# Kernel tuning notes

Hardware: AMD Instinct MI355X
Metric: run time of the kernel (lower is better)

## Reference

```python
import jax, jax.numpy as jnp
import numpy as np

NG, NC = 4096, 4096
FIN_G, FIN_C, D = 512, 512, 256
ALPHA = 0.2
NEG = -9.0e15

def leaky(x):
    return jnp.where(x >= 0, x, ALPHA * x)

def setup_inputs() -> dict:
    key = jax.random.key(0)
    ks = jax.random.split(key, 16)
    gene_x = jax.random.normal(ks[0], (NG, FIN_G), jnp.float32)
    cell_x = jax.random.normal(ks[1], (NC, FIN_C), jnp.float32)
    gene_adj = (jax.random.uniform(ks[2], (NG, NG)) < 0.05).astype(jnp.float32)
    gene_adj = jnp.maximum(gene_adj, jnp.eye(NG, dtype=jnp.float32))
    cell_adj = (jax.random.uniform(ks[3], (NC, NC)) < 0.05).astype(jnp.float32)
    cell_adj = jnp.maximum(cell_adj, jnp.eye(NC, dtype=jnp.float32))
    gene_cell_adj = (jax.random.uniform(ks[4], (NG, NC)) < 0.05).astype(jnp.float32)
    s = 1.414 * np.sqrt(6.0)
    def xav(k, shape):
        lim = s / np.sqrt(shape[0] + shape[1])
        return jax.random.uniform(k, shape, jnp.float32, -lim, lim)
    Wg = xav(ks[5], (D, FIN_G))
    Wc = xav(ks[6], (D, FIN_C))
    a_gg = xav(ks[7], (2 * D, 1))
    a_gc = xav(ks[8], (2 * D, 1))
    a_cc = xav(ks[9], (2 * D, 1))
    a_cg = xav(ks[10], (2 * D, 1))
    gate_g_w = xav(ks[11], (1, D))
    gate_c_w = xav(ks[12], (1, D))
    gate_g_b = jnp.full((1,), -2.0, jnp.float32)
    gate_c_b = jnp.full((1,), -2.0, jnp.float32)
    return dict(gene_x=gene_x, cell_x=cell_x, gene_adj=gene_adj, cell_adj=cell_adj,
                gene_cell_adj=gene_cell_adj, Wg=Wg, Wc=Wc, a_gg=a_gg, a_gc=a_gc,
                a_cc=a_cc, a_cg=a_cg, gate_g_w=gate_g_w, gate_g_b=gate_g_b,
                gate_c_w=gate_c_w, gate_c_b=gate_c_b)

def _gat_block(src_h, dst_h, a, adj):
    # attention of src rows over dst columns; adj: [Ns, Nd]
    d = src_h.shape[1]
    s1 = src_h @ a[:d, :]          # [Ns,1]
    s2 = dst_h @ a[d:, :]          # [Nd,1]
    e = leaky(s1 + s2.T)           # [Ns,Nd]
    att = jax.nn.softmax(jnp.where(adj > 0, e, NEG), axis=1)
    return att @ dst_h             # [Ns,d]

def reference(gene_x, cell_x, gene_adj, cell_adj, gene_cell_adj,
              Wg, Wc, a_gg, a_gc, a_cc, a_cg,
              gate_g_w, gate_g_b, gate_c_w, gate_c_b):
    gene_h = gene_x @ Wg.T   # [Ng,D]
    cell_h = cell_x @ Wc.T   # [Nc,D]
    gene_from_gene = _gat_block(gene_h, gene_h, a_gg, gene_adj)
    gene_from_cell = _gat_block(gene_h, cell_h, a_gc, gene_cell_adj)
    cell_from_cell = _gat_block(cell_h, cell_h, a_cc, cell_adj)
    cell_from_gene = _gat_block(cell_h, gene_h, a_cg, gene_cell_adj.T)
    gamma_g = jax.nn.sigmoid(gene_h @ gate_g_w.T + gate_g_b)  # [Ng,1]
    gamma_c = jax.nn.sigmoid(cell_h @ gate_c_w.T + gate_c_b)  # [Nc,1]
    gene_out = leaky(gene_h + gene_from_gene + gamma_g * gene_from_cell)
    cell_out = leaky(cell_h + cell_from_cell + gamma_c * cell_from_gene)
    return gene_out, cell_out
```

## Files before the change

kernel.cpp:

```cpp
#include <hip/hip_runtime.h>
#include <stdint.h>

#define NGC 4096
#define FIN 512
#define DD  256

typedef __attribute__((ext_vector_type(8))) short short8;
typedef __attribute__((ext_vector_type(4))) float f32x4;
typedef unsigned short u16;
typedef unsigned int   u32;
typedef unsigned long long u64;

static __device__ __forceinline__ float bf2f(u16 u){ return __uint_as_float(((u32)u)<<16); }
static __device__ __forceinline__ u16 f2bf(float f){
  u32 u = __float_as_uint(f);
  u += 0x7fffu + ((u>>16)&1u);
  return (u16)(u>>16);
}
static __device__ __forceinline__ u64 pack4bf(f32x4 v){
  u64 r;
  r  = (u64)f2bf(v[0]);
  r |= (u64)f2bf(v[1]) << 16;
  r |= (u64)f2bf(v[2]) << 32;
  r |= (u64)f2bf(v[3]) << 48;
  return r;
}
static __device__ __forceinline__ float lk(float x){ return fmaxf(x, 0.2f*x); }
static __device__ __forceinline__ u64 shfl_xor64(u64 x, int m){
  u32 lo = (u32)x, hi = (u32)(x >> 32);
  lo = __shfl_xor(lo, m); hi = __shfl_xor(hi, m);
  return ((u64)hi << 32) | lo;
}
static __device__ __forceinline__ u64 spread4(u64 x){
  x &= 0xFFFFull;
  x = (x | (x << 24)) & 0x000000FF000000FFull;
  x = (x | (x << 12)) & 0x000F000F000F000Full;
  x = (x | (x << 6))  & 0x0303030303030303ull;
  x = (x | (x << 3))  & 0x1111111111111111ull;
  return x;
}
static __device__ __forceinline__ void gl16(const void* g, void* l){
  __builtin_amdgcn_global_load_lds(
    (const __attribute__((address_space(1))) void*)g,
    (__attribute__((address_space(3))) void*)l, 16, 0, 0);
}

__global__ __launch_bounds__(256) void k_wcvt(
    const float* __restrict__ Wg, const float* __restrict__ Wc,
    u16* __restrict__ Wgbf, u16* __restrict__ Wcbf)
{
  int base = (blockIdx.x*256 + threadIdx.x)*4;
  float4 a = *(const float4*)(Wg + base);
  float4 b = *(const float4*)(Wc + base);
  ushort4 oa, ob;
  oa.x=f2bf(a.x); oa.y=f2bf(a.y); oa.z=f2bf(a.z); oa.w=f2bf(a.w);
  ob.x=f2bf(b.x); ob.y=f2bf(b.y); ob.z=f2bf(b.z); ob.w=f2bf(b.w);
  *(ushort4*)(Wgbf + base) = oa;
  *(ushort4*)(Wcbf + base) = ob;
}

__global__ __launch_bounds__(256) void k_pack(
    const float* __restrict__ gene_adj, const float* __restrict__ cell_adj,
    const float* __restrict__ gc_adj,   u64* __restrict__ packbits)
{
  int t = threadIdx.x, wid = t>>6, lane = t&63;
  int w = blockIdx.x*4 + wid;
  int row0 = w*6;
  const int sel = lane >> 2;
  const int sh = (lane & 3) * 16;

  float4 bufA[16], bufB[16];

  {
    int m = row0 >> 12;
    const float* sp = (m==0) ? gene_adj : (m==1) ? cell_adj : gc_adj;
    const float* rp = sp + (size_t)(row0 & 4095)*NGC + lane*4;
    #pragma unroll
    for(int j=0;j<16;j++) bufA[j] = *(const float4*)(rp + j*256);
  }

  #pragma unroll
  for(int i=0;i<6;i++){
    const bool evn = (i & 1) == 0;
    if(i < 5){
      int row = row0 + i + 1;
      int m = row >> 12;
      const float* sp = (m==0) ? gene_adj : (m==1) ? cell_adj : gc_adj;
      const float* rp = sp + (size_t)(row & 4095)*NGC + lane*4;
      if(evn){
        #pragma unroll
        for(int j=0;j<16;j++) bufB[j] = *(const float4*)(rp + j*256);
      } else {
        #pragma unroll
        for(int j=0;j<16;j++) bufA[j] = *(const float4*)(rp + j*256);
      }
    }
    u64 k0=0, k1=0, k2=0, k3=0;
    #pragma unroll
    for(int j=0;j<16;j++){
      float4 v = evn ? bufA[j] : bufB[j];
      u64 b0 = __ballot(v.x != 0.0f);
      u64 b1 = __ballot(v.y != 0.0f);
      u64 b2 = __ballot(v.z != 0.0f);
      u64 b3 = __ballot(v.w != 0.0f);
      if(sel == j){ k0=b0; k1=b1; k2=b2; k3=b3; }
    }
    u64 wv = spread4(k0 >> sh) | (spread4(k1 >> sh) << 1)
           | (spread4(k2 >> sh) << 2) | (spread4(k3 >> sh) << 3);
    int row = row0 + i;
    packbits[((size_t)(row >> 12) << 18) + (size_t)(row & 4095)*64 + lane] = wv;
  }
}

__global__ __launch_bounds__(256) void k_bitTT(
    const u64* __restrict__ gcb, u64* __restrict__ bT)
{
  int t = threadIdx.x, wid = t>>6, lane = t&63;
  int id = blockIdx.x*4 + wid;
  int G = id & 63, C = id >> 6;

  u64 x = gcb[(size_t)(64*G + lane)*64 + C];

  const u64 M1  = 0xAAAAAAAAAAAAAAAAull;
  const u64 M2  = 0xCCCCCCCCCCCCCCCCull;
  const u64 M4  = 0xF0F0F0F0F0F0F0F0ull;
  const u64 M8  = 0xFF00FF00FF00FF00ull;
  const u64 M16 = 0xFFFF0000FFFF0000ull;
  const u64 M32 = 0xFFFFFFFF00000000ull;
  #define TSTEP(S, M) { u64 y = shfl_xor64(x, S); \
    x = (lane & S) ? ((x & (M)) | ((y >> S) & ~(M))) \
                   : ((x & ~(M)) | ((y << S) & (M))); }
  TSTEP(32, M32) TSTEP(16, M16) TSTEP(8, M8)
  TSTEP(4,  M4)  TSTEP(2,  M2)  TSTEP(1, M1)
  #undef TSTEP

  bT[(size_t)(64*C + lane)*64 + G] = x;
}

__global__ __launch_bounds__(512) void k_hgemm(
    const float* __restrict__ xg, const float* __restrict__ xc,
    const u16* __restrict__ Wg, const u16* __restrict__ Wc,
    float* __restrict__ hg, float* __restrict__ hc,
    u16* __restrict__ hTg, u16* __restrict__ hTc)
{
  const int side = blockIdx.y;
  const float* x = side ? xc : xg;
  const u16* W = side ? Wc : Wg;
  float* h  = side ? hc : hg;
  u16*  hT  = side ? hTc : hTg;
  const int r0 = blockIdx.x * 64;
  const int t = threadIdx.x;
  const int wid = t >> 6, lane = t & 63;
  const int lrow = lane & 15, lhi = lane >> 4;

  __shared__ __align__(16) char smem[32768];

  f32x4 acc[4][2];
  const f32x4 z4 = {0.f,0.f,0.f,0.f};
  #pragma unroll
  for(int i=0;i<4;i++){ acc[i][0]=z4; acc[i][1]=z4; }

  const int r = t >> 3, c8 = t & 7;
  for(int k0 = 0; k0 < FIN; k0 += 64){
    const float* xp = x + (size_t)(r0 + r)*FIN + k0 + c8*8;
    float4 xa = *(const float4*)xp;
    float4 xb = *(const float4*)(xp + 4);
    short8 xv;
    xv[0]=(short)f2bf(xa.x); xv[1]=(short)f2bf(xa.y);
    xv[2]=(short)f2bf(xa.z); xv[3]=(short)f2bf(xa.w);
    xv[4]=(short)f2bf(xb.x); xv[5]=(short)f2bf(xb.y);
    xv[6]=(short)f2bf(xb.z); xv[7]=(short)f2bf(xb.w);
    int wbyte = r*128 + (((c8 ^ (r & 7)) & 7) << 4);
    *(short8*)(smem + wbyte) = xv;
    __syncthreads();
    #pragma unroll
    for(int ksub = 0; ksub < 2; ksub++){
      short8 b[2];
      #pragma unroll
      for(int nf=0; nf<2; nf++){
        int n = wid*32 + nf*16 + lrow;
        b[nf] = *(const short8*)(W + (size_t)n*FIN + k0 + ksub*32 + lhi*8);
      }
      #pragma unroll
      for(int mf=0; mf<4; mf++){
        int row = mf*16 + lrow;
        int g = ksub*4 + lhi;
        short8 a = *(const short8*)(smem + row*128 + (((g ^ (row & 7)) & 7) << 4));
        #pragma unroll
        for(int nf=0; nf<2; nf++)
          acc[mf][nf] = __builtin_amdgcn_mfma_f32_16x16x32_bf16(a, b[nf], acc[mf][nf], 0,0,0);
      }
    }
    __syncthreads();
  }
  #pragma unroll
  for(int mf=0; mf<4; mf++){
    #pragma unroll
    for(int nf=0; nf<2; nf++){
      int col = wid*32 + nf*16 + lrow;
      #pragma unroll
      for(int j=0;j<4;j++){
        int row = mf*16 + lhi*4 + j;
        float v = acc[mf][nf][j];
        h[(size_t)(r0+row)*DD + col] = v;
        int byte_ = col*128 + (((row*2) ^ ((col & 7)<<4)));
        *(u16*)(smem + byte_) = f2bf(v);
      }
    }
  }
  __syncthreads();
  {
    int n = t >> 1, half = t & 1;
    #pragma unroll
    for(int gi=0; gi<4; gi++){
      int g = half*4 + gi;
      int byte_ = n*128 + (((g ^ (n & 7)) & 7) << 4);
      short8 v = *(const short8*)(smem + byte_);
      int kcol = r0 + g*8;
      size_t off = (size_t)(kcol>>5)*8192 + (size_t)(n>>4)*512
                 + ((kcol>>3)&3)*128 + (n&15)*8;
      *(short8*)(hT + off) = v;
    }
  }
}

__global__ __launch_bounds__(256) void k_svec(
    const float* __restrict__ hg, const float* __restrict__ hc,
    const float* __restrict__ a_gg, const float* __restrict__ a_gc,
    const float* __restrict__ a_cc, const float* __restrict__ a_cg,
    const float* __restrict__ gw_g, const float* __restrict__ gb_g,
    const float* __restrict__ gw_c, const float* __restrict__ gb_c,
    float* __restrict__ sbuf)
{
  int t = threadIdx.x, wid = t>>6, lane = t&63;
  int idx = blockIdx.x * 4 + wid;
  int side = idx >> 12;
  int row  = idx & 4095;
  const float* h = (side ? hc : hg) + (size_t)row*DD;
  const float* v0 = (side ? a_cc : a_gg);
  const float* v1 = (side ? a_cc : a_gg) + DD;
  const float* v2 = (side ? a_cg : a_gc);
  const float* v3 = (side ? a_gc : a_cg) + DD;
  const float* gw = side ? gw_c : gw_g;
  float bias = (side ? gb_c : gb_g)[0];

  float4 hv = *(const float4*)(h + lane*4);
  float4 w0 = *(const float4*)(v0 + lane*4);
  float4 w1 = *(const float4*)(v1 + lane*4);
  float4 w2 = *(const float4*)(v2 + lane*4);
  float4 w3 = *(const float4*)(v3 + lane*4);
  float4 w4 = *(const float4*)(gw + lane*4);

  float d0 = hv.x*w0.x + hv.y*w0.y + hv.z*w0.z + hv.w*w0.w;
  float d1 = hv.x*w1.x + hv.y*w1.y + hv.z*w1.z + hv.w*w1.w;
  float d2 = hv.x*w2.x + hv.y*w2.y + hv.z*w2.z + hv.w*w2.w;
  float d3 = hv.x*w3.x + hv.y*w3.y + hv.z*w3.z + hv.w*w3.w;
  float d4 = hv.x*w4.x + hv.y*w4.y + hv.z*w4.z + hv.w*w4.w;
  #pragma unroll
  for(int s=1;s<64;s<<=1){
    d0 += __shfl_xor(d0, s); d1 += __shfl_xor(d1, s); d2 += __shfl_xor(d2, s);
    d3 += __shfl_xor(d3, s); d4 += __shfl_xor(d4, s);
  }
  if(lane == 0){
    float gam = 1.f/(1.f + __expf(-(d4 + bias)));
    if(side == 0){
      sbuf[0*4096+row]=d0; sbuf[1*4096+row]=d1; sbuf[2*4096+row]=d2;
      sbuf[3*4096+row]=d3; sbuf[4*4096+row]=gam;
    } else {
      sbuf[5*4096+row]=d0; sbuf[6*4096+row]=d1; sbuf[8*4096+row]=d2;
      sbuf[7*4096+row]=d3; sbuf[9*4096+row]=gam;
    }
  }
}

__global__ __launch_bounds__(256,2) void k_gat(
    const float* __restrict__ sbuf,
    const uint8_t* __restrict__ packbits, const uint8_t* __restrict__ bitsT,
    const u16* __restrict__ hTg, const u16* __restrict__ hTc,
    u16* __restrict__ part, float* __restrict__ Zpart)
{
  const int mode = blockIdx.z;
  const int kc   = blockIdx.y;
  const int nodebase = blockIdx.x * 64;
  const int kcbase   = kc * 2048;

  const float* s1; const float* s2; const uint8_t* bits; const u16* hT;
  if(mode == 0){ s1 = sbuf;        s2 = sbuf+4096;   bits = packbits;           hT = hTg; }
  else if(mode == 1){ s1 = sbuf+2*4096; s2 = sbuf+7*4096; bits = packbits+4194304; hT = hTc; }
  else if(mode == 2){ s1 = sbuf+5*4096; s2 = sbuf+6*4096; bits = packbits+2097152; hT = hTc; }
  else { s1 = sbuf+8*4096; s2 = sbuf+3*4096; bits = bitsT; hT = hTg; }

  const int t = threadIdx.x, wid = t>>6, lane = t&63, lrow = lane&15, lhi = lane>>4;
  const int kh = wid >> 1;
  const int ng_sub = wid & 1;

  __shared__ __align__(16) char U[81920];
  char* A_lds  = U;
  char* mask_l = U + 65536;

  {
    int row = t>>2, seg = t&3;
    const char* g = (const char*)bits + (size_t)(nodebase+row)*512 + kc*256 + seg*64;
    char* drow_ = mask_l + row*256;
    #pragma unroll
    for(int i=0;i<4;i++){
      int slot = seg*4 + i;
      *(ulonglong2*)(drow_ + (((slot ^ (row&7)))<<4)) = *(const ulonglong2*)(g + i*16);
    }
  }
  const char* hTb = (const char*)hT;
  {
    const char* g = hTb + ((size_t)kc*64 + kh*32 + 0)*16384 + ng_sub*8192 + lane*16;
    char* l = A_lds + 0*32768 + kh*16384 + ng_sub*8192;
    #pragma unroll
    for(int i=0;i<8;i++) gl16(g + i*1024, l + i*1024);
  }
  float mxv = -1e30f;
  #pragma unroll
  for(int i=0;i<16;i++){
    float4 v = *(const float4*)(s2 + lane*64 + i*4);
    mxv = fmaxf(mxv, fmaxf(fmaxf(v.x,v.y), fmaxf(v.z,v.w)));
  }
  #pragma unroll
  for(int sh=1; sh<64; sh<<=1) mxv = fmaxf(mxv, __shfl_xor(mxv, sh));
  const float maxs2 = mxv;

  const int wnode = nodebase + ng_sub*32;
  const float L2E = 1.4426950408889634f;
  float c1[2], c2[2], z[2];
  #pragma unroll
  for(int nf=0; nf<2; nf++){
    float s1v = s1[wnode + nf*16 + lrow];
    float m = lk(s1v + maxs2);
    c1[nf] = (s1v - m)*L2E;
    c2[nf] = (0.2f*s1v - m)*L2E;
    z[nf] = 0.f;
  }

  f32x4 acc[16][2];
  const f32x4 zz = {0.f,0.f,0.f,0.f};
  #pragma unroll
  for(int i=0;i<16;i++){ acc[i][0]=zz; acc[i][1]=zz; }

  const float* s2g = s2 + kcbase + kh*1024 + lhi*8;
  const char* mrow0 = mask_l + (ng_sub*32 + lrow)*256;
  const char* mrow1 = mask_l + (ng_sub*32 + 16 + lrow)*256;
  const int mx0 = (ng_sub*32 + lrow) & 7, mx1 = (ng_sub*32 + 16 + lrow) & 7;

  float4 csA = *(const float4*)(s2g);
  float4 csB = *(const float4*)(s2g + 4);

  __syncthreads();

  #pragma unroll 1
  for(int s=0; s<32; s++){
    const int cur = s & 1;
    if(s < 31){
      const char* g = hTb + ((size_t)kc*64 + kh*32 + s + 1)*16384 + ng_sub*8192 + lane*16;
      char* l = A_lds + (cur^1)*32768 + kh*16384 + ng_sub*8192;
      #pragma unroll
      for(int i=0;i<8;i++) gl16(g + i*1024, l + i*1024);
    }
    float4 sA = csA, sB = csB;
    if(s < 31){
      csA = *(const float4*)(s2g + (s+1)*32);
      csB = *(const float4*)(s2g + (s+1)*32 + 4);
    }
    float e1[8], e2[8];
    {
      float sv[8] = {sA.x,sA.y,sA.z,sA.w,sB.x,sB.y,sB.z,sB.w};
      #pragma unroll
      for(int j=0;j<8;j++){ e1[j] = sv[j]*L2E; e2[j] = sv[j]*(0.2f*L2E); }
    }
    const int slot = kh*8 + (s>>2), win = (s&3)*4;
    u32 mw0 = *(const u32*)(mrow0 + ((slot ^ mx0)<<4) + win);
    u32 mw1 = *(const u32*)(mrow1 + ((slot ^ mx1)<<4) + win);
    short8 b[2];
    #pragma unroll
    for(int nf=0; nf<2; nf++){
      u32 mw = nf ? mw1 : mw0;
      u32 w4[4];
      #pragma unroll
      for(int pr=0; pr<4; pr++){
        float bit0 = (float)((mw >> (lhi*8 + 2*pr  )) & 1u);
        float bit1 = (float)((mw >> (lhi*8 + 2*pr+1)) & 1u);
        float p0 = __builtin_amdgcn_exp2f(fmaxf(c1[nf]+e1[2*pr  ], c2[nf]+e2[2*pr  ])) * bit0;
        float p1 = __builtin_amdgcn_exp2f(fmaxf(c1[nf]+e1[2*pr+1], c2[nf]+e2[2*pr+1])) * bit1;
        z[nf] += p0 + p1;
        u32 q0 = __float_as_uint(p0) + 0x8000u;
        u32 q1 = __float_as_uint(p1) + 0x8000u;
        w4[pr] = (q1 & 0xFFFF0000u) | (q0 >> 16);
      }
      union{ u32 u[4]; short8 s8; } cv;
      cv.u[0]=w4[0]; cv.u[1]=w4[1]; cv.u[2]=w4[2]; cv.u[3]=w4[3];
      b[nf] = cv.s8;
    }
    const char* Af = A_lds + cur*32768 + kh*16384 + lane*16;
    #pragma unroll
    for(int mf=0; mf<16; mf++){
      short8 a = *(const short8*)(Af + mf*1024);
      acc[mf][0] = __builtin_amdgcn_mfma_f32_16x16x32_bf16(a, b[0], acc[mf][0], 0,0,0);
      acc[mf][1] = __builtin_amdgcn_mfma_f32_16x16x32_bf16(a, b[1], acc[mf][1], 0,0,0);
    }
    __syncthreads();
  }

  #pragma unroll
  for(int nf=0; nf<2; nf++){
    z[nf] += __shfl_xor(z[nf], 16);
    z[nf] += __shfl_xor(z[nf], 32);
  }
  if(lhi == 0){
    float* zp = Zpart + (size_t)(mode*4 + kc*2 + kh)*4096 + wnode;
    zp[lrow]      = z[0];
    zp[16 + lrow] = z[1];
  }

  __syncthreads();
  float* R = (float*)A_lds;
  u16* po = part + ((size_t)(mode*2 + kc) << 20);
  #pragma unroll
  for(int half=0; half<2; half++){
    if(kh == 1){
      #pragma unroll
      for(int mf8=0; mf8<8; mf8++){
        #pragma unroll
        for(int nf=0; nf<2; nf++){
          int r = ng_sub*32 + nf*16 + lrow;
          int byte_ = r*512 + ((mf8*64 + lhi*16) ^ ((r&7)<<4));
          *(f32x4*)((char*)R + byte_) = acc[half*8 + mf8][nf];
        }
      }
    }
    __syncthreads();
    if(kh == 0){
      #pragma unroll
      for(int mf8=0; mf8<8; mf8++){
        #pragma unroll
        for(int nf=0; nf<2; nf++){
          int r = ng_sub*32 + nf*16 + lrow;
          int byte_ = r*512 + ((mf8*64 + lhi*16) ^ ((r&7)<<4));
          f32x4 o = *(const f32x4*)((const char*)R + byte_);
          o = o + acc[half*8 + mf8][nf];
          int node = nodebase + r;
          *(u64*)(po + (size_t)node*256 + (half*8+mf8)*16 + lhi*4) = pack4bf(o);
        }
      }
    }
    __syncthreads();
  }
}

__global__ __launch_bounds__(256) void k_epi(
    const float* __restrict__ hg, const float* __restrict__ hc,
    const u16* __restrict__ part, const float* __restrict__ Zpart,
    const float* __restrict__ sbuf, float* __restrict__ out)
{
  int idx = blockIdx.x*256 + threadIdx.x;
  int fid = idx*4;
  int side = fid >> 20;
  int l = fid & 1048575;
  int node = l >> 8;
  int modeA = side ? 2 : 0, modeB = side ? 3 : 1;
  const float* h = side ? hc : hg;
  float gam = sbuf[(side ? 9 : 4)*4096 + node];
  float za = Zpart[(size_t)(modeA*4+0)*4096 + node] + Zpart[(size_t)(modeA*4+1)*4096 + node]
           + Zpart[(size_t)(modeA*4+2)*4096 + node] + Zpart[(size_t)(modeA*4+3)*4096 + node];
  float zb = Zpart[(size_t)(modeB*4+0)*4096 + node] + Zpart[(size_t)(modeB*4+1)*4096 + node]
           + Zpart[(size_t)(modeB*4+2)*4096 + node] + Zpart[(size_t)(modeB*4+3)*4096 + node];
  float rza = 1.f / fmaxf(za, 1e-30f);
  float rzb = 1.f / fmaxf(zb, 1e-30f);
  ushort4 a0 = *(const ushort4*)(part + ((size_t)(modeA*2  )<<20) + l);
  ushort4 a1 = *(const ushort4*)(part + ((size_t)(modeA*2+1)<<20) + l);
  ushort4 b0 = *(const ushort4*)(part + ((size_t)(modeB*2  )<<20) + l);
  ushort4 b1 = *(const ushort4*)(part + ((size_t)(modeB*2+1)<<20) + l);
  float4 h4 = *(const float4*)(h + l);
  float4 o;
  o.x = lk(h4.x + (bf2f(a0.x)+bf2f(a1.x))*rza + gam*(bf2f(b0.x)+bf2f(b1.x))*rzb);
  o.y = lk(h4.y + (bf2f(a0.y)+bf2f(a1.y))*rza + gam*(bf2f(b0.y)+bf2f(b1.y))*rzb);
  o.z = lk(h4.z + (bf2f(a0.z)+bf2f(a1.z))*rza + gam*(bf2f(b0.z)+bf2f(b1.z))*rzb);
  o.w = lk(h4.w + (bf2f(a0.w)+bf2f(a1.w))*rza + gam*(bf2f(b0.w)+bf2f(b1.w))*rzb);
  *(float4*)(out + fid) = o;
}

extern "C" void kernel_launch(void* const* d_in, const int* in_sizes, int n_in,
                              void* d_out, int out_size, void* d_ws, size_t ws_size,
                              hipStream_t stream)
{
  const float* gene_x   = (const float*)d_in[0];
  const float* cell_x   = (const float*)d_in[1];
  const float* gene_adj = (const float*)d_in[2];
  const float* cell_adj = (const float*)d_in[3];
  const float* gc_adj   = (const float*)d_in[4];
  const float* Wg       = (const float*)d_in[5];
  const float* Wc       = (const float*)d_in[6];
  const float* a_gg     = (const float*)d_in[7];
  const float* a_gc     = (const float*)d_in[8];
  const float* a_cc     = (const float*)d_in[9];
  const float* a_cg     = (const float*)d_in[10];
  const float* gw_g     = (const float*)d_in[11];
  const float* gb_g     = (const float*)d_in[12];
  const float* gw_c     = (const float*)d_in[13];
  const float* gb_c     = (const float*)d_in[14];

  char* ws = (char*)d_ws;
  float* hg   = (float*)(ws);
  float* hc   = (float*)(ws + (4u<<20));
  u16*   hTg  = (u16*)  (ws + (8u<<20));
  u16*   hTc  = (u16*)  (ws + (10u<<20));
  float* sbuf = (float*)(ws + (12u<<20));
  float* Zpart= (float*)(ws + (12u<<20) + (512u<<10));
  uint8_t* bitsT = (uint8_t*)(ws + (13u<<20));
  u16*   Wgbf = (u16*)  (ws + (17u<<20));
  u16*   Wcbf = (u16*)  (ws + (17u<<20) + (512u<<10));
  u16*   part = (u16*)  (ws + (17u<<20));
  u64*   packbits = (u64*)(ws + (49u<<20));

  k_wcvt<<<dim3(128), 256, 0, stream>>>(Wg, Wc, Wgbf, Wcbf);
  k_pack<<<dim3(512), 256, 0, stream>>>(gene_adj, cell_adj, gc_adj, packbits);
  k_bitTT<<<dim3(1024), 256, 0, stream>>>(packbits + 524288, (u64*)bitsT);
  k_hgemm<<<dim3(64,2), 512, 0, stream>>>(gene_x, cell_x, Wgbf, Wcbf, hg, hc, hTg, hTc);
  k_svec<<<dim3(2048), 256, 0, stream>>>(hg, hc, a_gg, a_gc, a_cc, a_cg,
                                         gw_g, gb_g, gw_c, gb_c, sbuf);
  k_gat<<<dim3(64,2,4), 256, 0, stream>>>(sbuf, (const uint8_t*)packbits,
                                          bitsT, hTg, hTc, part, Zpart);
  k_epi<<<dim3(2048), 256, 0, stream>>>(hg, hc, part, Zpart, sbuf, (float*)d_out);
}
```

Before: 133.8 us.

## Fuse adjacency packing and projection GEMM into one front kernel, convert W inline

Merges the adjacency bit-packing kernel and the feature projection GEMM into a single launch, with blocks 0-255 packing bits and blocks 256-383 computing h = xW^T. The separate fp32-to-bf16 weight conversion kernel is removed, and weights are now loaded as fp32 and converted inside the GEMM inner loop. This drops two launches and lets the memory-bound packing overlap with the GEMM. In exchange, every GEMM block redundantly converts W and reads twice as many weight bytes, and the fused kernel may need more registers.

```diff
diff --git a/kernel.cpp b/kernel.cpp
--- a/kernel.cpp
+++ b/kernel.cpp
@@ -45,115 +45,74 @@
     (__attribute__((address_space(3))) void*)l, 16, 0, 0);
 }
 
-__global__ __launch_bounds__(256) void k_wcvt(
-    const float* __restrict__ Wg, const float* __restrict__ Wc,
-    u16* __restrict__ Wgbf, u16* __restrict__ Wcbf)
-{
-  int base = (blockIdx.x*256 + threadIdx.x)*4;
-  float4 a = *(const float4*)(Wg + base);
-  float4 b = *(const float4*)(Wc + base);
-  ushort4 oa, ob;
-  oa.x=f2bf(a.x); oa.y=f2bf(a.y); oa.z=f2bf(a.z); oa.w=f2bf(a.w);
-  ob.x=f2bf(b.x); ob.y=f2bf(b.y); ob.z=f2bf(b.z); ob.w=f2bf(b.w);
-  *(ushort4*)(Wgbf + base) = oa;
-  *(ushort4*)(Wcbf + base) = ob;
-}
-
-__global__ __launch_bounds__(256) void k_pack(
+__global__ __launch_bounds__(512) void k_front(
     const float* __restrict__ gene_adj, const float* __restrict__ cell_adj,
-    const float* __restrict__ gc_adj,   u64* __restrict__ packbits)
-{
-  int t = threadIdx.x, wid = t>>6, lane = t&63;
-  int w = blockIdx.x*4 + wid;
-  int row0 = w*6;
-  const int sel = lane >> 2;
-  const int sh = (lane & 3) * 16;
-
-  float4 bufA[16], bufB[16];
-
-  {
-    int m = row0 >> 12;
-    const float* sp = (m==0) ? gene_adj : (m==1) ? cell_adj : gc_adj;
-    const float* rp = sp + (size_t)(row0 & 4095)*NGC + lane*4;
-    #pragma unroll
-    for(int j=0;j<16;j++) bufA[j] = *(const float4*)(rp + j*256);
-  }
-
-  #pragma unroll
-  for(int i=0;i<6;i++){
-    const bool evn = (i & 1) == 0;
-    if(i < 5){
-      int row = row0 + i + 1;
-      int m = row >> 12;
-      const float* sp = (m==0) ? gene_adj : (m==1) ? cell_adj : gc_adj;
-      const float* rp = sp + (size_t)(row & 4095)*NGC + lane*4;
-      if(evn){
-        #pragma unroll
-        for(int j=0;j<16;j++) bufB[j] = *(const float4*)(rp + j*256);
-      } else {
-        #pragma unroll
-        for(int j=0;j<16;j++) bufA[j] = *(const float4*)(rp + j*256);
-      }
-    }
-    u64 k0=0, k1=0, k2=0, k3=0;
-    #pragma unroll
-    for(int j=0;j<16;j++){
-      float4 v = evn ? bufA[j] : bufB[j];
-      u64 b0 = __ballot(v.x != 0.0f);
-      u64 b1 = __ballot(v.y != 0.0f);
-      u64 b2 = __ballot(v.z != 0.0f);
-      u64 b3 = __ballot(v.w != 0.0f);
-      if(sel == j){ k0=b0; k1=b1; k2=b2; k3=b3; }
-    }
-    u64 wv = spread4(k0 >> sh) | (spread4(k1 >> sh) << 1)
-           | (spread4(k2 >> sh) << 2) | (spread4(k3 >> sh) << 3);
-    int row = row0 + i;
-    packbits[((size_t)(row >> 12) << 18) + (size_t)(row & 4095)*64 + lane] = wv;
-  }
-}
-
-__global__ __launch_bounds__(256) void k_bitTT(
-    const u64* __restrict__ gcb, u64* __restrict__ bT)
-{
-  int t = threadIdx.x, wid = t>>6, lane = t&63;
-  int id = blockIdx.x*4 + wid;
-  int G = id & 63, C = id >> 6;
-
-  u64 x = gcb[(size_t)(64*G + lane)*64 + C];
-
-  const u64 M1  = 0xAAAAAAAAAAAAAAAAull;
-  const u64 M2  = 0xCCCCCCCCCCCCCCCCull;
-  const u64 M4  = 0xF0F0F0F0F0F0F0F0ull;
-  const u64 M8  = 0xFF00FF00FF00FF00ull;
-  const u64 M16 = 0xFFFF0000FFFF0000ull;
-  const u64 M32 = 0xFFFFFFFF00000000ull;
-  #define TSTEP(S, M) { u64 y = shfl_xor64(x, S); \
-    x = (lane & S) ? ((x & (M)) | ((y >> S) & ~(M))) \
-                   : ((x & ~(M)) | ((y << S) & (M))); }
-  TSTEP(32, M32) TSTEP(16, M16) TSTEP(8, M8)
-  TSTEP(4,  M4)  TSTEP(2,  M2)  TSTEP(1, M1)
-  #undef TSTEP
-
-  bT[(size_t)(64*C + lane)*64 + G] = x;
-}
-
-__global__ __launch_bounds__(512) void k_hgemm(
+    const float* __restrict__ gc_adj,   u64* __restrict__ packbits,
     const float* __restrict__ xg, const float* __restrict__ xc,
-    const u16* __restrict__ Wg, const u16* __restrict__ Wc,
+    const float* __restrict__ Wgf, const float* __restrict__ Wcf,
     float* __restrict__ hg, float* __restrict__ hc,
     u16* __restrict__ hTg, u16* __restrict__ hTc)
 {
-  const int side = blockIdx.y;
+  __shared__ __align__(16) char smem[32768];
+  const int t = threadIdx.x;
+  const int wid = t >> 6, lane = t & 63;
+
+  if(blockIdx.x < 256){
+    int w = blockIdx.x*8 + wid;
+    int row0 = w*6;
+    const int sel = lane >> 2;
+    const int sh = (lane & 3) * 16;
+
+    float4 bufA[16], bufB[16];
+    {
+      int m = row0 >> 12;
+      const float* sp = (m==0) ? gene_adj : (m==1) ? cell_adj : gc_adj;
+      const float* rp = sp + (size_t)(row0 & 4095)*NGC + lane*4;
+      #pragma unroll
+      for(int j=0;j<16;j++) bufA[j] = *(const float4*)(rp + j*256);
+    }
+    #pragma unroll
+    for(int i=0;i<6;i++){
+      const bool evn = (i & 1) == 0;
+      if(i < 5){
+        int row = row0 + i + 1;
+        int m = row >> 12;
+        const float* sp = (m==0) ? gene_adj : (m==1) ? cell_adj : gc_adj;
+        const float* rp = sp + (size_t)(row & 4095)*NGC + lane*4;
+        if(evn){
+          #pragma unroll
+          for(int j=0;j<16;j++) bufB[j] = *(const float4*)(rp + j*256);
+        } else {
+          #pragma unroll
+          for(int j=0;j<16;j++) bufA[j] = *(const float4*)(rp + j*256);
+        }
+      }
+      u64 k0=0, k1=0, k2=0, k3=0;
+      #pragma unroll
+      for(int j=0;j<16;j++){
+        float4 v = evn ? bufA[j] : bufB[j];
+        u64 b0 = __ballot(v.x != 0.0f);
+        u64 b1 = __ballot(v.y != 0.0f);
+        u64 b2 = __ballot(v.z != 0.0f);
+        u64 b3 = __ballot(v.w != 0.0f);
+        if(sel == j){ k0=b0; k1=b1; k2=b2; k3=b3; }
+      }
+      u64 wv = spread4(k0 >> sh) | (spread4(k1 >> sh) << 1)
+             | (spread4(k2 >> sh) << 2) | (spread4(k3 >> sh) << 3);
+      int row = row0 + i;
+      packbits[((size_t)(row >> 12) << 18) + (size_t)(row & 4095)*64 + lane] = wv;
+    }
+    return;
+  }
+
+  const int bid = blockIdx.x - 256;
+  const int side = bid >> 6;
   const float* x = side ? xc : xg;
-  const u16* W = side ? Wc : Wg;
+  const float* Wf = side ? Wcf : Wgf;
   float* h  = side ? hc : hg;
   u16*  hT  = side ? hTc : hTg;
-  const int r0 = blockIdx.x * 64;
-  const int t = threadIdx.x;
-  const int wid = t >> 6, lane = t & 63;
+  const int r0 = (bid & 63) * 64;
   const int lrow = lane & 15, lhi = lane >> 4;
-
-  __shared__ __align__(16) char smem[32768];
 
   f32x4 acc[4][2];
   const f32x4 z4 = {0.f,0.f,0.f,0.f};
@@ -179,7 +138,15 @@
       #pragma unroll
       for(int nf=0; nf<2; nf++){
         int n = wid*32 + nf*16 + lrow;
-        b[nf] = *(const short8*)(W + (size_t)n*FIN + k0 + ksub*32 + lhi*8);
+        const float* wp = Wf + (size_t)n*FIN + k0 + ksub*32 + lhi*8;
+        float4 wa = *(const float4*)wp;
+        float4 wb = *(const float4*)(wp + 4);
+        short8 bb;
+        bb[0]=(short)f2bf(wa.x); bb[1]=(short)f2bf(wa.y);
+        bb[2]=(short)f2bf(wa.z); bb[3]=(short)f2bf(wa.w);
+        bb[4]=(short)f2bf(wb.x); bb[5]=(short)f2bf(wb.y);
+        bb[6]=(short)f2bf(wb.z); bb[7]=(short)f2bf(wb.w);
+        b[nf] = bb;
       }
       #pragma unroll
       for(int mf=0; mf<4; mf++){
@@ -222,6 +189,31 @@
       *(short8*)(hT + off) = v;
     }
   }
+}
+
+__global__ __launch_bounds__(256) void k_bitTT(
+    const u64* __restrict__ gcb, u64* __restrict__ bT)
+{
+  int t = threadIdx.x, wid = t>>6, lane = t&63;
+  int id = blockIdx.x*4 + wid;
+  int G = id & 63, C = id >> 6;
+
+  u64 x = gcb[(size_t)(64*G + lane)*64 + C];
+
+  const u64 M1  = 0xAAAAAAAAAAAAAAAAull;
+  const u64 M2  = 0xCCCCCCCCCCCCCCCCull;
+  const u64 M4  = 0xF0F0F0F0F0F0F0F0ull;
+  const u64 M8  = 0xFF00FF00FF00FF00ull;
+  const u64 M16 = 0xFFFF0000FFFF0000ull;
+  const u64 M32 = 0xFFFFFFFF00000000ull;
+  #define TSTEP(S, M) { u64 y = shfl_xor64(x, S); \
+    x = (lane & S) ? ((x & (M)) | ((y >> S) & ~(M))) \
+                   : ((x & ~(M)) | ((y << S) & (M))); }
+  TSTEP(32, M32) TSTEP(16, M16) TSTEP(8, M8)
+  TSTEP(4,  M4)  TSTEP(2,  M2)  TSTEP(1, M1)
+  #undef TSTEP
+
+  bT[(size_t)(64*C + lane)*64 + G] = x;
 }
 
 __global__ __launch_bounds__(256) void k_svec(
@@ -511,15 +503,13 @@
   float* sbuf = (float*)(ws + (12u<<20));
   float* Zpart= (float*)(ws + (12u<<20) + (512u<<10));
   uint8_t* bitsT = (uint8_t*)(ws + (13u<<20));
-  u16*   Wgbf = (u16*)  (ws + (17u<<20));
-  u16*   Wcbf = (u16*)  (ws + (17u<<20) + (512u<<10));
   u16*   part = (u16*)  (ws + (17u<<20));
   u64*   packbits = (u64*)(ws + (49u<<20));
 
-  k_wcvt<<<dim3(128), 256, 0, stream>>>(Wg, Wc, Wgbf, Wcbf);
-  k_pack<<<dim3(512), 256, 0, stream>>>(gene_adj, cell_adj, gc_adj, packbits);
+  k_front<<<dim3(384), 512, 0, stream>>>(gene_adj, cell_adj, gc_adj, packbits,
+                                         gene_x, cell_x, Wg, Wc,
+                                         hg, hc, hTg, hTc);
   k_bitTT<<<dim3(1024), 256, 0, stream>>>(packbits + 524288, (u64*)bitsT);
-  k_hgemm<<<dim3(64,2), 512, 0, stream>>>(gene_x, cell_x, Wgbf, Wcbf, hg, hc, hTg, hTc);
   k_svec<<<dim3(2048), 256, 0, stream>>>(hg, hc, a_gg, a_gc, a_cc, a_cg,
                                          gw_g, gb_g, gw_c, gb_c, sbuf);
   k_gat<<<dim3(64,2,4), 256, 0, stream>>>(sbuf, (const uint8_t*)packbits,
```

Measured after the change: 132.9 us (median of 2 runs). About the same (-0.6%).
